# Kernel tuning notes

Measured on AMD Instinct MI355X. Metric: run time of the kernel, lower is better.

The kernel has to match this reference:

```python
import jax, jax.numpy as jnp
import numpy as np

N_QUBITS = 14
N_LAYERS = 3
BATCH = 256


def _apply_1q(state, U, q, n):
    # state: (B, 2^n) flat; apply 2x2 gate U on qubit q.
    # U: (2,2) shared or (B,2,2) per-sample.
    B = state.shape[0]
    s = state.reshape(B, 2 ** q, 2, 2 ** (n - 1 - q))
    if U.ndim == 3:
        s = jnp.einsum('bij,bajc->baic', U, s)
    else:
        s = jnp.einsum('ij,bajc->baic', U, s)
    return s.reshape(B, -1)


def _apply_cnot(state, c, t, n):
    # CNOT: |c, t> -> |c, t xor c>. Flip target axis on the control=1 block.
    B = state.shape[0]
    a, b = (c, t) if c < t else (t, c)
    s = state.reshape(B, 2 ** a, 2, 2 ** (b - a - 1), 2, 2 ** (n - 1 - b))
    c_ax = 2 if c < t else 4
    t_ax = 4 if c < t else 2
    s0 = jax.lax.index_in_dim(s, 0, axis=c_ax, keepdims=False)
    s1 = jax.lax.index_in_dim(s, 1, axis=c_ax, keepdims=False)
    t_ax2 = t_ax if t_ax < c_ax else t_ax - 1
    s1 = jnp.flip(s1, axis=t_ax2)
    s = jnp.stack([s0, s1], axis=c_ax)
    return s.reshape(B, -1)


def _circuit(x, weights, n, L):
    # angles constrained to (-pi, pi) as in the torch wrapper
    angles = jnp.tanh(x) * jnp.float32(np.pi)  # (B, n)
    B = x.shape[0]
    state = jnp.zeros((B, 2 ** n), jnp.complex64).at[:, 0].set(1.0)
    # AngleEmbedding with RY rotations (per-sample gate matrices)
    for q in range(n):
        th = angles[:, q] * 0.5
        c, s = jnp.cos(th), jnp.sin(th)
        U = jnp.stack([jnp.stack([c, -s], -1), jnp.stack([s, c], -1)], -2)
        state = _apply_1q(state, U.astype(jnp.complex64), q, n)
    # BasicEntanglerLayers: per layer, RX(w) on each wire then CNOT ring
    for l in range(L):
        for q in range(n):
            th = weights[l, q] * 0.5
            c = jnp.cos(th).astype(jnp.complex64)
            s = jnp.sin(th).astype(jnp.complex64)
            mis = jnp.complex64(-1j) * s
            U = jnp.stack([jnp.stack([c, mis]), jnp.stack([mis, c])])
            state = _apply_1q(state, U, q, n)
        num_cnots = n if n > 2 else (1 if n == 2 else 0)
        for q in range(num_cnots):
            state = _apply_cnot(state, q, (q + 1) % n, n)
    # <Z_q> = P(q=0) - P(q=1)
    p = (jnp.abs(state) ** 2).reshape((B,) + (2,) * n)  # float32 probs
    expvals = []
    for q in range(n):
        pq = jnp.sum(p, axis=tuple(a for a in range(1, n + 1) if a != q + 1))
        expvals.append(pq[:, 0] - pq[:, 1])
    return jnp.stack(expvals, axis=-1)  # (B, n)


def setup_inputs() -> dict:
    key = jax.random.key(0)
    kx, kw = jax.random.split(key)
    x = jax.random.normal(kx, (BATCH, N_QUBITS), jnp.float32)
    # TorchLayer default init for BasicEntanglerLayers: uniform in [0, 2*pi)
    weights = jax.random.uniform(kw, (N_LAYERS, N_QUBITS), jnp.float32, 0.0, 2.0 * np.pi)
    return {"x": x, "weights": weights}


def reference(x, weights):
    return _circuit(x, weights, N_QUBITS, N_LAYERS)
```

## Files before the change

### kernel.cpp

```cpp
#include <hip/hip_runtime.h>
#include <math.h>

#define NQ 14
#define DIM (1 << NQ)
#define NT 512
#define TA 32
#define NW (NT / 64)
#define PDIM (DIM + DIM / 32)

template <int J> struct IC { static constexpr int v = J; };
template <int N, typename F>
__device__ __forceinline__ void sfor(F&& f) {
    if constexpr (N > 0) { sfor<N - 1>(f); f(IC<N - 1>{}); }
}

typedef float cf2 __attribute__((ext_vector_type(2)));

__device__ __forceinline__ cf2 pk_mul_c(cf2 cs, cf2 a) {
    cf2 t;
    asm("v_pk_mul_f32 %0, %1, %2 op_sel:[0,0] op_sel_hi:[0,1]"
        : "=v"(t) : "v"(cs), "v"(a));
    return t;
}
__device__ __forceinline__ cf2 pk_mul_s(cf2 cs, cf2 a) {
    cf2 t;
    asm("v_pk_mul_f32 %0, %1, %2 op_sel:[1,0] op_sel_hi:[1,1]"
        : "=v"(t) : "v"(cs), "v"(a));
    return t;
}
__device__ __forceinline__ cf2 pk_mul_s_swapneg(cf2 cs, cf2 a) {
    cf2 t;
    asm("v_pk_mul_f32 %0, %1, %2 op_sel:[1,1] op_sel_hi:[1,0] neg_hi:[0,1]"
        : "=v"(t) : "v"(cs), "v"(a));
    return t;
}
__device__ __forceinline__ cf2 pk_fma_c(cf2 cs, cf2 a, cf2 b) {
    cf2 d;
    asm("v_pk_fma_f32 %0, %1, %2, %3 op_sel:[0,0,0] op_sel_hi:[0,1,1]"
        : "=v"(d) : "v"(cs), "v"(a), "v"(b));
    return d;
}
__device__ __forceinline__ cf2 pk_fma_s(cf2 cs, cf2 a, cf2 b) {
    cf2 d;
    asm("v_pk_fma_f32 %0, %1, %2, %3 op_sel:[1,0,0] op_sel_hi:[1,1,1]"
        : "=v"(d) : "v"(cs), "v"(a), "v"(b));
    return d;
}
__device__ __forceinline__ cf2 pk_fma_c_nb(cf2 cs, cf2 a, cf2 b) {
    cf2 d;
    asm("v_pk_fma_f32 %0, %1, %2, %3 op_sel:[0,0,0] op_sel_hi:[0,1,1] neg_lo:[0,0,1] neg_hi:[0,0,1]"
        : "=v"(d) : "v"(cs), "v"(a), "v"(b));
    return d;
}

struct St {
    cf2 a0, a1, a2, a3, a4, a5, a6, a7, a8, a9, a10, a11, a12, a13, a14, a15,
        a16, a17, a18, a19, a20, a21, a22, a23, a24, a25, a26, a27, a28, a29, a30, a31;
};
template <int J> __device__ __forceinline__ cf2& amp(St& s);
#define AMP_GET(J) template <> __device__ __forceinline__ cf2& amp<J>(St& s) { return s.a##J; }
AMP_GET(0)  AMP_GET(1)  AMP_GET(2)  AMP_GET(3)  AMP_GET(4)  AMP_GET(5)  AMP_GET(6)  AMP_GET(7)
AMP_GET(8)  AMP_GET(9)  AMP_GET(10) AMP_GET(11) AMP_GET(12) AMP_GET(13) AMP_GET(14) AMP_GET(15)
AMP_GET(16) AMP_GET(17) AMP_GET(18) AMP_GET(19) AMP_GET(20) AMP_GET(21) AMP_GET(22) AMP_GET(23)
AMP_GET(24) AMP_GET(25) AMP_GET(26) AMP_GET(27) AMP_GET(28) AMP_GET(29) AMP_GET(30) AMP_GET(31)

__host__ __device__ constexpr int pad(int idx) { return idx + (idx >> 5); }

template <int P0, int P1, int P2, int P3, int P4>
struct Tile5 {
    static constexpr int PMASK = (1 << P0) | (1 << P1) | (1 << P2) | (1 << P3) | (1 << P4);
    static __device__ __forceinline__ int base_idx(int t) {
        int idx = 0, tb = 0;
#pragma unroll
        for (int p = 0; p < NQ; ++p)
            if (!((PMASK >> p) & 1)) { idx |= ((t >> tb) & 1) << p; ++tb; }
        return idx;
    }
    static constexpr int off(int j) {
        return ((j & 1) << P0) | (((j >> 1) & 1) << P1) | (((j >> 2) & 1) << P2) |
               (((j >> 3) & 1) << P3) | (((j >> 4) & 1) << P4);
    }
    static constexpr int poff(int j) { return pad(off(j)); }
};

using TT1 = Tile5<9, 10, 11, 12, 13>;
using TT2 = Tile5<4, 5, 6, 7, 8>;
using TT3 = Tile5<13, 0, 1, 2, 3>;

template <class T>
__device__ __forceinline__ void load_tile(const cf2* s, int pb, St& st) {
    sfor<TA>([&](auto jc) {
        constexpr int j0 = decltype(jc)::v;
        constexpr int j = (j0 >> 1) | ((j0 & 1) << 4);
        amp<j>(st) = s[pb + T::poff(j)];
    });
}
template <class T>
__device__ __forceinline__ void load_tile_fold(const cf2* s, int pbLo, int pbHi, St& st) {
    sfor<TA>([&](auto jc) {
        constexpr int j0 = decltype(jc)::v;
        constexpr int j = (j0 >> 1) | ((j0 & 1) << 4);
        amp<j>(st) = s[((j & 16) ? pbHi : pbLo) + T::poff(j)];
    });
}
template <class T, int HI>
__device__ __forceinline__ void store_half(cf2* s, int pb, St& st) {
    sfor<TA>([&](auto jc) {
        constexpr int j = decltype(jc)::v;
        if constexpr ((j >> 4) == HI) s[pb + T::poff(j)] = amp<j>(st);
    });
}

template <int LB>
__device__ __forceinline__ void g_ry(St& st, cf2 cs) {
    sfor<TA>([&](auto jc) {
        constexpr int j = decltype(jc)::v;
        if constexpr (!(j & (1 << LB))) {
            constexpr int k = j | (1 << LB);
            cf2 aj = amp<j>(st), ak = amp<k>(st);
            amp<j>(st) = pk_fma_c_nb(cs, aj, pk_mul_s(cs, ak));
            amp<k>(st) = pk_fma_s(cs, aj, pk_mul_c(cs, ak));
        }
    });
}
template <int LB>
__device__ __forceinline__ void g_rx(St& st, cf2 cs) {
    sfor<TA>([&](auto jc) {
        constexpr int j = decltype(jc)::v;
        if constexpr (!(j & (1 << LB))) {
            constexpr int k = j | (1 << LB);
            cf2 aj = amp<j>(st), ak = amp<k>(st);
            amp<j>(st) = pk_fma_c(cs, aj, pk_mul_s_swapneg(cs, ak));
            amp<k>(st) = pk_fma_c(cs, ak, pk_mul_s_swapneg(cs, aj));
        }
    });
}
template <int LB, int HI>
__device__ __forceinline__ void g_ry_h(St& st, cf2 cs) {
    sfor<TA>([&](auto jc) {
        constexpr int j = decltype(jc)::v;
        if constexpr (!(j & (1 << LB)) && ((j >> 4) == HI)) {
            constexpr int k = j | (1 << LB);
            cf2 aj = amp<j>(st), ak = amp<k>(st);
            amp<j>(st) = pk_fma_c_nb(cs, aj, pk_mul_s(cs, ak));
            amp<k>(st) = pk_fma_s(cs, aj, pk_mul_c(cs, ak));
        }
    });
}
template <int LB, int HI>
__device__ __forceinline__ void g_rx_h(St& st, cf2 cs) {
    sfor<TA>([&](auto jc) {
        constexpr int j = decltype(jc)::v;
        if constexpr (!(j & (1 << LB)) && ((j >> 4) == HI)) {
            constexpr int k = j | (1 << LB);
            cf2 aj = amp<j>(st), ak = amp<k>(st);
            amp<j>(st) = pk_fma_c(cs, aj, pk_mul_s_swapneg(cs, ak));
            amp<k>(st) = pk_fma_c(cs, ak, pk_mul_s_swapneg(cs, aj));
        }
    });
}
template <int LC, int LT, int HI>
__device__ __forceinline__ void g_cnot_h(St& st) {
    sfor<TA>([&](auto jc) {
        constexpr int j = decltype(jc)::v;
        if constexpr (((j >> LC) & 1) && !((j >> LT) & 1) && ((j >> 4) == HI)) {
            constexpr int k = j | (1 << LT);
            cf2 t = amp<j>(st);
            amp<j>(st) = amp<k>(st);
            amp<k>(st) = t;
        }
    });
}
template <int LT>
__device__ __forceinline__ void g_cnot_pred(St& st, bool ctrl) {
    sfor<TA>([&](auto jc) {
        constexpr int j = decltype(jc)::v;
        if constexpr (!((j >> LT) & 1)) {
            constexpr int k = j | (1 << LT);
            cf2 a = amp<j>(st), b = amp<k>(st);
            amp<j>(st) = ctrl ? b : a;
            amp<k>(st) = ctrl ? a : b;
        }
    });
}

__global__ void __launch_bounds__(NT) qsim_kernel(const float* __restrict__ x,
                                                  const float* __restrict__ w,
                                                  float* __restrict__ out) {
    __shared__ cf2 sSt[PDIM];
    __shared__ cf2 sCS[56];
    __shared__ float sRed[NW][NQ];

    const int tid = threadIdx.x;
    const int b = blockIdx.x;

    if (tid < 14) {
        float th = tanhf(x[b * NQ + tid]) * 1.57079632679489662f;
        cf2 v; v.x = cosf(th); v.y = sinf(th);
        sCS[tid] = v;
    } else if (tid < 56) {
        float th = w[tid - 14] * 0.5f;
        cf2 v; v.x = cosf(th); v.y = sinf(th);
        sCS[tid] = v;
    }

    const int pbT1 = pad(TT1::base_idx(tid));
    const int pbT2 = pad(TT2::base_idx(tid));
    const int pbT3 = pad(TT3::base_idx(tid));
    const int d2 = ((tid >> 4) & 1) ? 264 : 0;
    const int pbT2lo = pbT2 + d2, pbT2hi = pbT2 - d2;
    const int d3 = (tid & 1) ? 8 : 0;
    const int pbT3lo = pbT3 + d3, pbT3hi = pbT3 - d3;

    const bool c45 = (tid >> 4) & 1;
    const bool c9A = tid & 1;

    __syncthreads();

    St st;

    {
        cf2 y5 = sCS[5], y6 = sCS[6], y7 = sCS[7], y8 = sCS[8], y9 = sCS[9];
        cf2 x5 = sCS[19], x6 = sCS[20], x7 = sCS[21], x8 = sCS[22], x9 = sCS[23];

        const int B0 = (tid >> 8) & 1, B1 = (tid >> 7) & 1, B2 = (tid >> 6) & 1,
                  B3 = (tid >> 5) & 1, B4 = (tid >> 4) & 1;
        const int bb0 = B0, bb1 = B1 ^ B0, bb2 = B2 ^ B1, bb3 = B3 ^ B2, bb4 = B4 ^ B3;
        const int bb[5] = {bb0, bb1, bb2, bb3, bb4};
        float pr = 1.f, pi = 0.f;
#pragma unroll
        for (int q = 0; q < 5; ++q) {
            cf2 ry = sCS[q], rx = sCS[14 + q];
            float re = bb[q] ? rx.x * ry.y : rx.x * ry.x;
            float im = bb[q] ? -rx.y * ry.x : -rx.y * ry.y;
            float nr = pr * re - pi * im;
            pi = pr * im + pi * re;
            pr = nr;
        }
        const bool act = (tid & 15) == 0;

        sfor<TA>([&](auto jc) {
            constexpr int j = decltype(jc)::v;
            cf2 z; z.x = 0.f; z.y = 0.f;
            amp<j>(st) = z;
        });
        amp<0>(st).x = act ? pr : 0.f;
        amp<0>(st).y = act ? pi : 0.f;

        g_ry<4>(st, y5); g_rx<4>(st, x5); g_cnot_pred<4>(st, c45);
        g_ry_h<3,0>(st, y6); g_ry_h<2,0>(st, y7); g_ry_h<1,0>(st, y8); g_ry_h<0,0>(st, y9);
        g_rx_h<3,0>(st, x6); g_rx_h<2,0>(st, x7); g_rx_h<1,0>(st, x8); g_rx_h<0,0>(st, x9);
        g_cnot_h<3,2,0>(st); g_cnot_h<2,1,0>(st); g_cnot_h<1,0,0>(st);
        store_half<TT2, 0>(sSt, pbT2, st);
        g_ry_h<3,1>(st, y6); g_ry_h<2,1>(st, y7); g_ry_h<1,1>(st, y8); g_ry_h<0,1>(st, y9);
        g_rx_h<3,1>(st, x6); g_rx_h<2,1>(st, x7); g_rx_h<1,1>(st, x8); g_rx_h<0,1>(st, x9);
        g_cnot_h<4,3,1>(st); g_cnot_h<3,2,1>(st); g_cnot_h<2,1,1>(st); g_cnot_h<1,0,1>(st);
        store_half<TT2, 1>(sSt, pbT2, st);
    }
    __syncthreads();
    {
        cf2 yA = sCS[10], yB = sCS[11], yC = sCS[12], yD = sCS[13];
        cf2 xA = sCS[24], xB = sCS[25], xC = sCS[26], xD = sCS[27];
        load_tile<TT3>(sSt, pbT3, st);
        g_ry<4>(st, yA); g_rx<4>(st, xA); g_cnot_pred<4>(st, c9A);
        g_ry_h<3,0>(st, yB); g_ry_h<2,0>(st, yC); g_ry_h<1,0>(st, yD);
        g_rx_h<3,0>(st, xB); g_rx_h<2,0>(st, xC); g_rx_h<1,0>(st, xD);
        g_cnot_h<3,2,0>(st); g_cnot_h<2,1,0>(st); g_cnot_h<1,0,0>(st);
        store_half<TT3, 0>(sSt, pbT3, st);
        g_ry_h<3,1>(st, yB); g_ry_h<2,1>(st, yC); g_ry_h<1,1>(st, yD);
        g_rx_h<3,1>(st, xB); g_rx_h<2,1>(st, xC); g_rx_h<1,1>(st, xD);
        g_cnot_h<4,3,1>(st); g_cnot_h<3,2,1>(st); g_cnot_h<2,1,1>(st); g_cnot_h<1,0,1>(st);
        store_half<TT3, 1>(sSt, pbT3, st);
    }
    __syncthreads();

#pragma unroll 1
    for (int l = 1; l < 3; ++l) {
        const int s0 = 14 + l * NQ;
        {
            cf2 c0 = sCS[s0 + 0], c1 = sCS[s0 + 1], c2 = sCS[s0 + 2];
            cf2 c3 = sCS[s0 + 3], c4 = sCS[s0 + 4];
            load_tile<TT1>(sSt, pbT1, st);
            g_rx<4>(st, c0);
            g_rx_h<3,0>(st, c1); g_rx_h<2,0>(st, c2); g_rx_h<1,0>(st, c3); g_rx_h<0,0>(st, c4);
            g_cnot_h<3,2,0>(st); g_cnot_h<2,1,0>(st); g_cnot_h<1,0,0>(st);
            store_half<TT1, 0>(sSt, pbT1, st);
            g_rx_h<3,1>(st, c1); g_rx_h<2,1>(st, c2); g_rx_h<1,1>(st, c3); g_rx_h<0,1>(st, c4);
            g_cnot_h<4,3,1>(st); g_cnot_h<3,2,1>(st); g_cnot_h<2,1,1>(st); g_cnot_h<1,0,1>(st);
            store_half<TT1, 1>(sSt, pbT1, st);
        }
        __syncthreads();
        {
            cf2 c5 = sCS[s0 + 5], c6 = sCS[s0 + 6], c7 = sCS[s0 + 7];
            cf2 c8 = sCS[s0 + 8], c9 = sCS[s0 + 9];
            load_tile_fold<TT2>(sSt, pbT2lo, pbT2hi, st);
            g_rx<4>(st, c5);
            g_rx_h<3,0>(st, c6); g_rx_h<2,0>(st, c7); g_rx_h<1,0>(st, c8); g_rx_h<0,0>(st, c9);
            g_cnot_h<3,2,0>(st); g_cnot_h<2,1,0>(st); g_cnot_h<1,0,0>(st);
            store_half<TT2, 0>(sSt, pbT2, st);
            g_rx_h<3,1>(st, c6); g_rx_h<2,1>(st, c7); g_rx_h<1,1>(st, c8); g_rx_h<0,1>(st, c9);
            g_cnot_h<4,3,1>(st); g_cnot_h<3,2,1>(st); g_cnot_h<2,1,1>(st); g_cnot_h<1,0,1>(st);
            store_half<TT2, 1>(sSt, pbT2, st);
        }
        __syncthreads();
        {
            cf2 cA = sCS[s0 + 10], cB = sCS[s0 + 11], cC = sCS[s0 + 12], cD = sCS[s0 + 13];
            load_tile_fold<TT3>(sSt, pbT3lo, pbT3hi, st);
            g_rx<4>(st, cA);
            g_rx_h<3,0>(st, cB); g_rx_h<2,0>(st, cC); g_rx_h<1,0>(st, cD);
            g_cnot_h<3,2,0>(st); g_cnot_h<2,1,0>(st); g_cnot_h<1,0,0>(st);
            if (l == 1) store_half<TT3, 0>(sSt, pbT3, st);
            g_rx_h<3,1>(st, cB); g_rx_h<2,1>(st, cC); g_rx_h<1,1>(st, cD);
            g_cnot_h<4,3,1>(st); g_cnot_h<3,2,1>(st); g_cnot_h<2,1,1>(st); g_cnot_h<1,0,1>(st);
            if (l == 1) store_half<TT3, 1>(sSt, pbT3, st);
        }
        if (l == 1) __syncthreads();
    }

    float Stot = 0.f, S0 = 0.f, S1 = 0.f, S2 = 0.f, S3 = 0.f, S4 = 0.f;
    sfor<TA>([&](auto jc) {
        constexpr int j = decltype(jc)::v;
        cf2 v = amp<j>(st);
        float pj = v.x * v.x + v.y * v.y;
        Stot += pj;
        S0 += (j & 1)  ? -pj : pj;
        S1 += (j & 2)  ? -pj : pj;
        S2 += (j & 4)  ? -pj : pj;
        S3 += (j & 8)  ? -pj : pj;
        S4 += (j & 16) ? -pj : pj;
    });
    float ev[NQ];
    ev[0] = S0; ev[10] = S4; ev[11] = S3; ev[12] = S2; ev[13] = S1;
#pragma unroll
    for (int q = 1; q <= 9; ++q)
        ev[q] = ((tid >> (9 - q)) & 1) ? -Stot : Stot;

#pragma unroll
    for (int q = 0; q < NQ; ++q) {
#pragma unroll
        for (int o = 32; o > 0; o >>= 1) ev[q] += __shfl_down(ev[q], o);
    }
    const int wv = tid >> 6, ln = tid & 63;
    if (ln == 0) {
#pragma unroll
        for (int q = 0; q < NQ; ++q) sRed[wv][q] = ev[q];
    }
    __syncthreads();
    if (tid < NQ) {
        float acc = 0.f;
#pragma unroll
        for (int k = 0; k < NW; ++k) acc += sRed[k][tid];
        out[b * NQ + tid] = acc;
    }
}

extern "C" void kernel_launch(void* const* d_in, const int* in_sizes, int n_in,
                              void* d_out, int out_size, void* d_ws, size_t ws_size,
                              hipStream_t stream) {
    const float* x = (const float*)d_in[0];
    const float* w = (const float*)d_in[1];
    float* out = (float*)d_out;
    qsim_kernel<<<256, NT, 0, stream>>>(x, w, out);
}
```

Before: 74.11 us.

## Compute first-layer state analytically as a product state, skipping two tile passes

The embedding RY layer and the first RX layer act on |0>, so the state after them is a product state. The kernel now builds each amplitude directly from per-qubit factors using complex multiplies, with the first-layer CNOT ring folded in as XOR relations on bit indices. It then applies only the layer-1 TT1 pass (RX on wires 0-4 plus the CNOTs) and stores the result. This removes the old TT2 and TT3 passes of layer 0, along with their shared-memory round-trips and one barrier. The loop skips the TT1 pass at l==1 because that pass has already been fused in, at the cost of more intricate index algebra.

```diff
diff --git a/kernel.cpp b/kernel.cpp
--- a/kernel.cpp
+++ b/kernel.cpp
@@ -16,18 +16,6 @@
 
 typedef float cf2 __attribute__((ext_vector_type(2)));
 
-__device__ __forceinline__ cf2 pk_mul_c(cf2 cs, cf2 a) {
-    cf2 t;
-    asm("v_pk_mul_f32 %0, %1, %2 op_sel:[0,0] op_sel_hi:[0,1]"
-        : "=v"(t) : "v"(cs), "v"(a));
-    return t;
-}
-__device__ __forceinline__ cf2 pk_mul_s(cf2 cs, cf2 a) {
-    cf2 t;
-    asm("v_pk_mul_f32 %0, %1, %2 op_sel:[1,0] op_sel_hi:[1,1]"
-        : "=v"(t) : "v"(cs), "v"(a));
-    return t;
-}
 __device__ __forceinline__ cf2 pk_mul_s_swapneg(cf2 cs, cf2 a) {
     cf2 t;
     asm("v_pk_mul_f32 %0, %1, %2 op_sel:[1,1] op_sel_hi:[1,0] neg_hi:[0,1]"
@@ -37,18 +25,6 @@
 __device__ __forceinline__ cf2 pk_fma_c(cf2 cs, cf2 a, cf2 b) {
     cf2 d;
     asm("v_pk_fma_f32 %0, %1, %2, %3 op_sel:[0,0,0] op_sel_hi:[0,1,1]"
-        : "=v"(d) : "v"(cs), "v"(a), "v"(b));
-    return d;
-}
-__device__ __forceinline__ cf2 pk_fma_s(cf2 cs, cf2 a, cf2 b) {
-    cf2 d;
-    asm("v_pk_fma_f32 %0, %1, %2, %3 op_sel:[1,0,0] op_sel_hi:[1,1,1]"
-        : "=v"(d) : "v"(cs), "v"(a), "v"(b));
-    return d;
-}
-__device__ __forceinline__ cf2 pk_fma_c_nb(cf2 cs, cf2 a, cf2 b) {
-    cf2 d;
-    asm("v_pk_fma_f32 %0, %1, %2, %3 op_sel:[0,0,0] op_sel_hi:[0,1,1] neg_lo:[0,0,1] neg_hi:[0,0,1]"
         : "=v"(d) : "v"(cs), "v"(a), "v"(b));
     return d;
 }
@@ -112,18 +88,6 @@
 }
 
 template <int LB>
-__device__ __forceinline__ void g_ry(St& st, cf2 cs) {
-    sfor<TA>([&](auto jc) {
-        constexpr int j = decltype(jc)::v;
-        if constexpr (!(j & (1 << LB))) {
-            constexpr int k = j | (1 << LB);
-            cf2 aj = amp<j>(st), ak = amp<k>(st);
-            amp<j>(st) = pk_fma_c_nb(cs, aj, pk_mul_s(cs, ak));
-            amp<k>(st) = pk_fma_s(cs, aj, pk_mul_c(cs, ak));
-        }
-    });
-}
-template <int LB>
 __device__ __forceinline__ void g_rx(St& st, cf2 cs) {
     sfor<TA>([&](auto jc) {
         constexpr int j = decltype(jc)::v;
@@ -136,18 +100,6 @@
     });
 }
 template <int LB, int HI>
-__device__ __forceinline__ void g_ry_h(St& st, cf2 cs) {
-    sfor<TA>([&](auto jc) {
-        constexpr int j = decltype(jc)::v;
-        if constexpr (!(j & (1 << LB)) && ((j >> 4) == HI)) {
-            constexpr int k = j | (1 << LB);
-            cf2 aj = amp<j>(st), ak = amp<k>(st);
-            amp<j>(st) = pk_fma_c_nb(cs, aj, pk_mul_s(cs, ak));
-            amp<k>(st) = pk_fma_s(cs, aj, pk_mul_c(cs, ak));
-        }
-    });
-}
-template <int LB, int HI>
 __device__ __forceinline__ void g_rx_h(St& st, cf2 cs) {
     sfor<TA>([&](auto jc) {
         constexpr int j = decltype(jc)::v;
@@ -171,17 +123,15 @@
         }
     });
 }
-template <int LT>
-__device__ __forceinline__ void g_cnot_pred(St& st, bool ctrl) {
-    sfor<TA>([&](auto jc) {
-        constexpr int j = decltype(jc)::v;
-        if constexpr (!((j >> LT) & 1)) {
-            constexpr int k = j | (1 << LT);
-            cf2 a = amp<j>(st), b = amp<k>(st);
-            amp<j>(st) = ctrl ? b : a;
-            amp<k>(st) = ctrl ? a : b;
-        }
-    });
+
+__device__ __forceinline__ cf2 cmul(cf2 a, cf2 b) {
+    cf2 r; r.x = a.x * b.x - a.y * b.y; r.y = a.x * b.y + a.y * b.x; return r;
+}
+__device__ __forceinline__ cf2 v_of(cf2 ry, cf2 rx, int b) {
+    cf2 r;
+    r.x = b ? rx.x * ry.y : rx.x * ry.x;
+    r.y = b ? -(rx.y * ry.x) : -(rx.y * ry.y);
+    return r;
 }
 
 __global__ void __launch_bounds__(NT) qsim_kernel(const float* __restrict__ x,
@@ -212,72 +162,74 @@
     const int d3 = (tid & 1) ? 8 : 0;
     const int pbT3lo = pbT3 + d3, pbT3hi = pbT3 - d3;
 
-    const bool c45 = (tid >> 4) & 1;
-    const bool c9A = tid & 1;
-
     __syncthreads();
 
     St st;
 
     {
-        cf2 y5 = sCS[5], y6 = sCS[6], y7 = sCS[7], y8 = sCS[8], y9 = sCS[9];
-        cf2 x5 = sCS[19], x6 = sCS[20], x7 = sCS[21], x8 = sCS[22], x9 = sCS[23];
-
-        const int B0 = (tid >> 8) & 1, B1 = (tid >> 7) & 1, B2 = (tid >> 6) & 1,
-                  B3 = (tid >> 5) & 1, B4 = (tid >> 4) & 1;
-        const int bb0 = B0, bb1 = B1 ^ B0, bb2 = B2 ^ B1, bb3 = B3 ^ B2, bb4 = B4 ^ B3;
-        const int bb[5] = {bb0, bb1, bb2, bb3, bb4};
-        float pr = 1.f, pi = 0.f;
-#pragma unroll
-        for (int q = 0; q < 5; ++q) {
-            cf2 ry = sCS[q], rx = sCS[14 + q];
-            float re = bb[q] ? rx.x * ry.y : rx.x * ry.x;
-            float im = bb[q] ? -rx.y * ry.x : -rx.y * ry.y;
-            float nr = pr * re - pi * im;
-            pi = pr * im + pi * re;
-            pr = nr;
-        }
-        const bool act = (tid & 15) == 0;
-
+        const int t0 = tid & 1,        t1 = (tid >> 1) & 1, t2 = (tid >> 2) & 1,
+                  t3 = (tid >> 3) & 1, t4 = (tid >> 4) & 1, t5 = (tid >> 5) & 1,
+                  t6 = (tid >> 6) & 1, t7 = (tid >> 7) & 1, t8 = (tid >> 8) & 1;
+        const int b6 = t7 ^ t8, b7 = t6 ^ t7, b8 = t5 ^ t6, b9 = t4 ^ t5;
+        const int b10 = t3 ^ t4, b11 = t2 ^ t3, b12 = t1 ^ t2, b13 = t0 ^ t1;
+        cf2 Pref = v_of(sCS[6], sCS[20], b6);
+        Pref = cmul(Pref, v_of(sCS[7],  sCS[21], b7));
+        Pref = cmul(Pref, v_of(sCS[8],  sCS[22], b8));
+        Pref = cmul(Pref, v_of(sCS[9],  sCS[23], b9));
+        Pref = cmul(Pref, v_of(sCS[10], sCS[24], b10));
+        Pref = cmul(Pref, v_of(sCS[11], sCS[25], b11));
+        Pref = cmul(Pref, v_of(sCS[12], sCS[26], b12));
+        Pref = cmul(Pref, v_of(sCS[13], sCS[27], b13));
+        cf2 w0[2] = { v_of(sCS[0], sCS[14], t0),     v_of(sCS[0], sCS[14], 1 ^ t0) };
+        cf2 w1[2] = { v_of(sCS[1], sCS[15], t0),     v_of(sCS[1], sCS[15], 1 ^ t0) };
+        cf2 v2[2] = { v_of(sCS[2], sCS[16], 0),      v_of(sCS[2], sCS[16], 1) };
+        cf2 v3[2] = { v_of(sCS[3], sCS[17], 0),      v_of(sCS[3], sCS[17], 1) };
+        cf2 v4[2] = { v_of(sCS[4], sCS[18], 0),      v_of(sCS[4], sCS[18], 1) };
+        cf2 w5[2] = { v_of(sCS[5], sCS[19], t8),     v_of(sCS[5], sCS[19], 1 ^ t8) };
+        cf2 u[4] = { cmul(v4[0], w5[0]), cmul(v4[1], w5[1]),
+                     cmul(v4[1], w5[0]), cmul(v4[0], w5[1]) };
+        cf2 tA[2], tB[4], tC[8], tD[16];
+        sfor<2>([&](auto ic) {
+            constexpr int i = decltype(ic)::v;
+            tA[i] = cmul(Pref, w0[i]);
+        });
+        sfor<4>([&](auto ic) {
+            constexpr int i = decltype(ic)::v;
+            constexpr int j4 = i >> 1, j3 = i & 1;
+            tB[i] = cmul(tA[j4], w1[j3 ^ j4]);
+        });
+        sfor<8>([&](auto ic) {
+            constexpr int i = decltype(ic)::v;
+            constexpr int j3 = (i >> 1) & 1, j2 = i & 1;
+            tC[i] = cmul(tB[i >> 1], v2[j2 ^ j3]);
+        });
+        sfor<16>([&](auto ic) {
+            constexpr int i = decltype(ic)::v;
+            constexpr int j2 = (i >> 1) & 1, j1 = i & 1;
+            tD[i] = cmul(tC[i >> 1], v3[j1 ^ j2]);
+        });
         sfor<TA>([&](auto jc) {
             constexpr int j = decltype(jc)::v;
-            cf2 z; z.x = 0.f; z.y = 0.f;
-            amp<j>(st) = z;
-        });
-        amp<0>(st).x = act ? pr : 0.f;
-        amp<0>(st).y = act ? pi : 0.f;
-
-        g_ry<4>(st, y5); g_rx<4>(st, x5); g_cnot_pred<4>(st, c45);
-        g_ry_h<3,0>(st, y6); g_ry_h<2,0>(st, y7); g_ry_h<1,0>(st, y8); g_ry_h<0,0>(st, y9);
-        g_rx_h<3,0>(st, x6); g_rx_h<2,0>(st, x7); g_rx_h<1,0>(st, x8); g_rx_h<0,0>(st, x9);
-        g_cnot_h<3,2,0>(st); g_cnot_h<2,1,0>(st); g_cnot_h<1,0,0>(st);
-        store_half<TT2, 0>(sSt, pbT2, st);
-        g_ry_h<3,1>(st, y6); g_ry_h<2,1>(st, y7); g_ry_h<1,1>(st, y8); g_ry_h<0,1>(st, y9);
-        g_rx_h<3,1>(st, x6); g_rx_h<2,1>(st, x7); g_rx_h<1,1>(st, x8); g_rx_h<0,1>(st, x9);
-        g_cnot_h<4,3,1>(st); g_cnot_h<3,2,1>(st); g_cnot_h<2,1,1>(st); g_cnot_h<1,0,1>(st);
-        store_half<TT2, 1>(sSt, pbT2, st);
-    }
-    __syncthreads();
-    {
-        cf2 yA = sCS[10], yB = sCS[11], yC = sCS[12], yD = sCS[13];
-        cf2 xA = sCS[24], xB = sCS[25], xC = sCS[26], xD = sCS[27];
-        load_tile<TT3>(sSt, pbT3, st);
-        g_ry<4>(st, yA); g_rx<4>(st, xA); g_cnot_pred<4>(st, c9A);
-        g_ry_h<3,0>(st, yB); g_ry_h<2,0>(st, yC); g_ry_h<1,0>(st, yD);
-        g_rx_h<3,0>(st, xB); g_rx_h<2,0>(st, xC); g_rx_h<1,0>(st, xD);
-        g_cnot_h<3,2,0>(st); g_cnot_h<2,1,0>(st); g_cnot_h<1,0,0>(st);
-        store_half<TT3, 0>(sSt, pbT3, st);
-        g_ry_h<3,1>(st, yB); g_ry_h<2,1>(st, yC); g_ry_h<1,1>(st, yD);
-        g_rx_h<3,1>(st, xB); g_rx_h<2,1>(st, xC); g_rx_h<1,1>(st, xD);
-        g_cnot_h<4,3,1>(st); g_cnot_h<3,2,1>(st); g_cnot_h<2,1,1>(st); g_cnot_h<1,0,1>(st);
-        store_half<TT3, 1>(sSt, pbT3, st);
+            constexpr int j0 = j & 1, j1 = (j >> 1) & 1;
+            amp<j>(st) = cmul(tD[j >> 1], u[(j1 << 1) | j0]);
+        });
+
+        g_rx<4>(st, sCS[28 + 0]);
+        g_rx_h<3, 0>(st, sCS[28 + 1]); g_rx_h<2, 0>(st, sCS[28 + 2]);
+        g_rx_h<1, 0>(st, sCS[28 + 3]); g_rx_h<0, 0>(st, sCS[28 + 4]);
+        g_cnot_h<3, 2, 0>(st); g_cnot_h<2, 1, 0>(st); g_cnot_h<1, 0, 0>(st);
+        store_half<TT1, 0>(sSt, pbT1, st);
+        g_rx_h<3, 1>(st, sCS[28 + 1]); g_rx_h<2, 1>(st, sCS[28 + 2]);
+        g_rx_h<1, 1>(st, sCS[28 + 3]); g_rx_h<0, 1>(st, sCS[28 + 4]);
+        g_cnot_h<4, 3, 1>(st); g_cnot_h<3, 2, 1>(st); g_cnot_h<2, 1, 1>(st); g_cnot_h<1, 0, 1>(st);
+        store_half<TT1, 1>(sSt, pbT1, st);
     }
     __syncthreads();
 
 #pragma unroll 1
     for (int l = 1; l < 3; ++l) {
         const int s0 = 14 + l * NQ;
-        {
+        if (l == 2) {
             cf2 c0 = sCS[s0 + 0], c1 = sCS[s0 + 1], c2 = sCS[s0 + 2];
             cf2 c3 = sCS[s0 + 3], c4 = sCS[s0 + 4];
             load_tile<TT1>(sSt, pbT1, st);
@@ -288,8 +240,8 @@
             g_rx_h<3,1>(st, c1); g_rx_h<2,1>(st, c2); g_rx_h<1,1>(st, c3); g_rx_h<0,1>(st, c4);
             g_cnot_h<4,3,1>(st); g_cnot_h<3,2,1>(st); g_cnot_h<2,1,1>(st); g_cnot_h<1,0,1>(st);
             store_half<TT1, 1>(sSt, pbT1, st);
-        }
-        __syncthreads();
+            __syncthreads();
+        }
         {
             cf2 c5 = sCS[s0 + 5], c6 = sCS[s0 + 6], c7 = sCS[s0 + 7];
             cf2 c8 = sCS[s0 + 8], c9 = sCS[s0 + 9];
```

Measured after the change: 71.00 us. 4.2% less time.
